# Kernel tuning notes

Hardware: AMD Instinct MI355X
Metric: run time of the kernel (lower is better)

The kernel has to match this reference:

```python
import jax, jax.numpy as jnp
import numpy as np

B, N, E, S, A, P, T = 512, 65536, 131072, 256, 512, 2, 64


def setup_inputs() -> dict:
    key = jax.random.key(0)
    ks = jax.random.split(key, 40)
    f32 = jnp.float32

    def g(i, shape, s=0.05):
        return jax.random.normal(ks[i], shape, f32) * s

    inp = {
        'nodes': jax.random.normal(ks[0], (N, S), f32),
        'edge_features': jax.random.normal(ks[1], (E, S), f32),
        'edge_source': jax.random.randint(ks[2], (E,), 0, N),
        'edge_dest': jax.random.randint(ks[3], (E,), 0, N),
        'node_owner': jax.random.randint(ks[4], (N,), 0, B),
        'running': jnp.ones((B,), bool),
        'ref_types': jax.random.randint(ks[5], (B,), 0, T),
        # decision aggregator (transform + sigmoid gate)
        'dec_t_W': g(6, (A, S)), 'dec_t_b': g(7, (A,)),
        'dec_g_W': g(8, (A, S)), 'dec_g_b': jnp.ones((A,), f32),
        # init aggregator
        'init_t_W': g(9, (A, S)), 'init_t_b': g(10, (A,)),
        'init_g_W': g(11, (A, S)), 'init_g_b': jnp.ones((A,), f32),
        # node type decision head + embedding
        'ntd_W': g(12, (T + 1, A)), 'ntd_b': g(13, (T + 1,)),
        'nte': g(14, (T, S), 1.0),
        # f_init
        'f1_W': g(15, (S, S)), 'f1_b': g(16, (S,)),
        'f2_W': g(17, (S, A)),
        # propagator params, stacked over P steps (message_size = 2S)
        'mn_W': g(18, (P, 2 * S, S)),
        'mf_W': g(19, (P, 2 * S, S)),
        'ml2_W': g(20, (P, 2 * S, 2 * S)), 'ml2_b': g(21, (P, 2 * S)),
        'gru_Wih': g(22, (P, 3 * S, 2 * S)), 'gru_Whh': g(23, (P, 3 * S, S)),
        'gru_bih': jnp.zeros((P, 3 * S), f32),
        'gru_bhh': jnp.concatenate(
            [jnp.ones((P, S), f32), jnp.zeros((P, 2 * S), f32)], axis=-1),
    }
    return inp


def _aggregate(nodes, fmask, tW, tb, gW, gb):
    # Aggregator.forward: sigmoid gate * linear transform, pooled per graph
    # via dense 0/1 owner-mask matmul (dropout=0 -> identity).
    gates = jax.nn.sigmoid(nodes @ gW.T + gb)
    data = nodes @ tW.T + tb
    return fmask @ (data * gates)  # [B, A]


def reference(nodes, edge_features, edge_source, edge_dest, node_owner,
              running, ref_types,
              dec_t_W, dec_t_b, dec_g_W, dec_g_b,
              init_t_W, init_t_b, init_g_W, init_g_b,
              ntd_W, ntd_b, nte, f1_W, f1_b, f2_W,
              mn_W, mf_W, ml2_W, ml2_b, gru_Wih, gru_Whh, gru_bih, gru_bhh):
    f32 = nodes.dtype
    fmask = (node_owner[None, :] == jnp.arange(B)[:, None]).astype(f32)  # [B,N]
    # Propagator._node_update_mask: owner_masks[running].sum(0) > 0
    upd = (fmask * running[:, None].astype(f32)).sum(0) > 0  # [N]

    for p in range(P):
        ef = edge_features @ mf_W[p].T                 # [E, 2S]
        nf = nodes @ mn_W[p].T                         # [N, 2S]
        msgs = nf[edge_source] + nf[edge_dest] + ef
        msgs = jnp.tanh(msgs) @ ml2_W[p].T + ml2_b[p]  # message_layer_2
        inputs = jnp.zeros((N, 2 * S), f32)
        inputs = inputs.at[edge_dest].add(msgs).at[edge_source].add(msgs)
        # torch GRUCell (gate order r, z, n)
        gi = inputs @ gru_Wih[p].T + gru_bih[p]
        gh = nodes @ gru_Whh[p].T + gru_bhh[p]
        ir, iz, inn = jnp.split(gi, 3, axis=-1)
        hr, hz, hn = jnp.split(gh, 3, axis=-1)
        r = jax.nn.sigmoid(ir + hr)
        z = jax.nn.sigmoid(iz + hz)
        n = jnp.tanh(inn + r * hn)
        new_nodes = (1.0 - z) * n + z * nodes
        nodes = jnp.where(upd[:, None], new_nodes, nodes)

    # node-type decision
    agg = _aggregate(nodes, fmask, dec_t_W, dec_t_b, dec_g_W, dec_g_b)
    logits = agg @ ntd_W.T + ntd_b                      # [B, T+1]

    # training path: remap_pad (no pad chars present) -> ref + 1
    sel = ref_types + 1                                  # in [1, T]
    logp = jax.nn.log_softmax(logits, axis=-1)
    per_ex = -logp[jnp.arange(B), sel]
    loss = jnp.where(running, per_ex, 0.0).mean()

    # new node features for running graphs
    emb = nte[sel - 1]                                   # [B, S]
    init_feats = _aggregate(nodes, fmask, init_t_W, init_t_b,
                            init_g_W, init_g_b)
    new_features = emb @ f1_W.T + f1_b + init_feats @ f2_W.T  # [B, S]
    return logits, new_features, loss
```

## Files before the change

### kernel.cpp

```cpp
#include <hip/hip_runtime.h>
#include <hip/hip_bf16.h>
#include <math.h>

#define BG 512
#define NN 65536
#define EE 131072
#define SD 256
#define AD 512
#define PP 2
#define TD 64

typedef __attribute__((ext_vector_type(8))) short sx8;
typedef __attribute__((ext_vector_type(4))) short sx4;
typedef __attribute__((ext_vector_type(4))) float fx4;

__device__ __forceinline__ float bs2f(short s) {
    union { unsigned u; float f; } x; x.u = ((unsigned)(unsigned short)s) << 16; return x.f;
}
__device__ __forceinline__ short f2bs(float f) {
    union { float f; unsigned u; } x; x.f = f;
    unsigned r = x.u + 0x7fffu + ((x.u >> 16) & 1u);
    return (short)(r >> 16);
}
__device__ __forceinline__ float fast_tanh(float x) {
    float xc = fminf(fmaxf(x, -15.f), 15.f);
    float e = __expf(2.f * xc);
    return __fdividef(e - 1.f, e + 1.f);
}
__device__ __forceinline__ float fast_sigm(float x) {
    float xc = fminf(fmaxf(x, -30.f), 30.f);
    float e = __expf(-xc);
    return __fdividef(1.f, 1.f + e);
}
__device__ __forceinline__ bool run_flag(const void* runv, int idx) {
    const unsigned char* r8 = (const unsigned char*)runv;
    const int* r32 = (const int*)runv;
    return (r8[idx] != 0) || (r32[idx] != 0);
}

__device__ __forceinline__ void gload16(const short* g, short* l) {
    __builtin_amdgcn_global_load_lds(
        (const __attribute__((address_space(1))) void*)g,
        (__attribute__((address_space(3))) void*)l, 16, 0, 0);
}

template<int EPI>
__launch_bounds__(256, 4)
__global__ void gemm_bt(const short* __restrict__ Abp, const short* __restrict__ Abp2,
                        const short* __restrict__ Wp,
                        const float* __restrict__ bias, const float* __restrict__ bias2,
                        short* __restrict__ Cout, short* __restrict__ Fout,
                        short* __restrict__ FoutB,
                        const float* __restrict__ biasB, const float* __restrict__ biasB2,
                        const int* __restrict__ degp,
                        int K, int Ksp, int NC, int NT, int nsplit)
{
    __shared__ __align__(16) short sA[2 * 4096];
    __shared__ __align__(16) short sB[2 * 4096];
    const int t = threadIdx.x;
    const int lane = t & 63;
    const int w = t >> 6;

    const int nwg = gridDim.x;
    const int q = nwg >> 3;
    const int wg = (blockIdx.x & 7) * q + (blockIdx.x >> 3);
    const int mt = wg / NT;
    const int nt = wg - mt * NT;
    const int m0 = mt * 128;
    const int n0 = nt * 128;

    const int wm = (w >> 1) * 64;
    const int wn = (w & 1) * 64;
    const int lr = lane & 15;
    const int lg = lane >> 4;

    fx4 acc[4][4];
#pragma unroll
    for (int i = 0; i < 4; i++)
#pragma unroll
        for (int j = 0; j < 4; j++) { fx4 z = {0.f, 0.f, 0.f, 0.f}; acc[i][j] = z; }

    const int r = t >> 2;
    const int cblk = (t & 3) ^ ((r >> 1) & 3);
    const short* gA  = Abp  + (size_t)(m0 + r) * Ksp + cblk * 8;
    const short* gA2 = Abp2 + (size_t)(m0 + r) * (K - Ksp) + cblk * 8;
    const short* gB  = Wp + (size_t)(n0 + r) * K + cblk * 8;
    const size_t rsA  = (size_t)64 * Ksp;
    const size_t rsA2 = (size_t)64 * (K - Ksp);
    const size_t rsB  = (size_t)64 * K;

    auto STAGE = [&](int b, int kk) {
        const short* a0 = (kk < Ksp) ? (gA + kk) : (gA2 + (kk - Ksp));
        const size_t rs = (kk < Ksp) ? rsA : rsA2;
        gload16(a0,            sA + b * 4096 + w * 512);
        gload16(a0 + rs,       sA + b * 4096 + 2048 + w * 512);
        gload16(gB + kk,       sB + b * 4096 + w * 512);
        gload16(gB + kk + rsB, sB + b * 4096 + 2048 + w * 512);
    };

    STAGE(0, 0);

    float dgv[4];
    if (EPI == 3) {
#pragma unroll
        for (int mi = 0; mi < 4; mi++)
            dgv[mi] = (float)degp[m0 + wm + mi * 16 + lr];
    }

    __syncthreads();
    int buf = 0;
    const int xa = (lr >> 1) & 3;
    for (int kk = 0; kk < K; kk += 32) {
        if (kk + 32 < K) STAGE(buf ^ 1, kk + 32);
        const short* cA = sA + buf * 4096;
        const short* cB = sB + buf * 4096;
        sx8 af[4], bfr[4];
#pragma unroll
        for (int mi = 0; mi < 4; mi++)
            af[mi] = *(const sx8*)(cA + (wm + mi * 16 + lr) * 32 + (lg ^ xa) * 8);
#pragma unroll
        for (int ni = 0; ni < 4; ni++)
            bfr[ni] = *(const sx8*)(cB + (wn + ni * 16 + lr) * 32 + (lg ^ xa) * 8);
#pragma unroll
        for (int mi = 0; mi < 4; mi++)
#pragma unroll
            for (int ni = 0; ni < 4; ni++) {
                if (EPI == 4)
                    acc[mi][ni] = __builtin_amdgcn_mfma_f32_16x16x32_bf16(
                        af[mi], bfr[ni], acc[mi][ni], 0, 0, 0);
                else
                    acc[mi][ni] = __builtin_amdgcn_mfma_f32_16x16x32_bf16(
                        bfr[ni], af[mi], acc[mi][ni], 0, 0, 0);
            }
        __syncthreads();
        buf ^= 1;
    }

    if (EPI == 4) {
        const bool useB = (n0 >= nsplit);
        short* fo = useB ? FoutB : Fout;
        const float* tb = useB ? biasB : bias;
        const float* gb = useB ? biasB2 : bias2;
        const int ln0 = useB ? (n0 - nsplit) : n0;
#pragma unroll
        for (int mi = 0; mi < 4; mi++) {
#pragma unroll
            for (int rg = 0; rg < 4; rg++) {
                const int m = m0 + wm + mi * 16 + lg * 4 + rg;
#pragma unroll
                for (int ni = 0; ni < 4; ni += 2) {
                    const int rc = (((ln0 + wn + ni * 16) >> 5) << 4) + lr;
                    float dv = acc[mi][ni][rg] + tb[rc];
                    float gv = fast_sigm(acc[mi][ni + 1][rg] + gb[rc]);
                    fo[(size_t)m * 512 + rc] = f2bs(dv * gv);
                }
            }
        }
    } else {
#pragma unroll
        for (int mi = 0; mi < 4; mi++) {
            const int m = m0 + wm + mi * 16 + lr;
            short* co = Cout + (size_t)m * NC + n0;
#pragma unroll
            for (int ni = 0; ni < 4; ni++) {
                const int nc = wn + ni * 16 + lg * 4;
                sx4 o;
                if (EPI == 1) {
#pragma unroll
                    for (int rg = 0; rg < 4; rg++)
                        o[rg] = f2bs(fast_tanh(acc[mi][ni][rg]));
                } else if (EPI == 3) {
                    fx4 bv = *(const fx4*)(bias + n0 + nc);
                    fx4 cv = *(const fx4*)(bias2 + n0 + nc);
#pragma unroll
                    for (int rg = 0; rg < 4; rg++)
                        o[rg] = f2bs(acc[mi][ni][rg] + dgv[mi] * cv[rg] + bv[rg]);
                } else {
                    fx4 vb = {0.f, 0.f, 0.f, 0.f};
                    if (bias) vb = *(const fx4*)(bias + n0 + nc);
#pragma unroll
                    for (int rg = 0; rg < 4; rg++)
                        o[rg] = f2bs(acc[mi][ni][rg] + vb[rg]);
                }
                *(sx4*)(co + nc) = o;
            }
        }
    }
}

__global__ void k_xadd(const short* __restrict__ nodes, const int* __restrict__ esrc,
                       const int* __restrict__ edst, short* __restrict__ X)
{
    size_t idx = ((size_t)blockIdx.x * 256 + threadIdx.x) * 8;
    const int e = (int)(idx >> 8);
    const int j = (int)(idx & 255);
    const int s = esrc[e], d = edst[e];
    sx8 a = *(const sx8*)(nodes + (size_t)s * 256 + j);
    sx8 b = *(const sx8*)(nodes + (size_t)d * 256 + j);
    sx8 o;
#pragma unroll
    for (int u = 0; u < 8; u++) o[u] = f2bs(bs2f(a[u]) + bs2f(b[u]));
    *(sx8*)(X + idx) = o;
}

__global__ void k_castw(const float* __restrict__ in, short* __restrict__ out)
{
    size_t i = ((size_t)blockIdx.x * 256 + threadIdx.x) * 4;
    fx4 v = *(const fx4*)(in + i);
    sx4 o;
#pragma unroll
    for (int u = 0; u < 4; u++) o[u] = f2bs(v[u]);
    *(sx4*)(out + i) = o;
}

__global__ void k_cast_T(const float* __restrict__ in, short* __restrict__ out)
{
    size_t i = ((size_t)blockIdx.x * 256 + threadIdx.x) * 4;
    const int k = (int)(i >> 9);
    const int k2 = (int)(i & 511);
    sx4 o;
#pragma unroll
    for (int u = 0; u < 4; u++) o[u] = f2bs(in[(size_t)(k2 + u) * 512 + k]);
    *(sx4*)(out + i) = o;
}

__global__ void k_vecfuse(const float* __restrict__ Wih, const float* __restrict__ ml2b,
                          float* __restrict__ c1)
{
    const int i = blockIdx.x * 256 + threadIdx.x;
    if (i >= 768) return;
    const float* wr = Wih + (size_t)i * 512;
    float acc = 0.f;
    for (int k = 0; k < 512; k++) acc += wr[k] * ml2b[k];
    c1[i] = acc;
}

__global__ void k_fill_gru(const short* __restrict__ Whh, short* __restrict__ out)
{
    size_t idx = ((size_t)blockIdx.x * 256 + threadIdx.x) * 4;
    const int o = (int)(idx / 768);
    const int k = (int)(idx % 768);
    if (o < 768 && k < 512) return;
    sx4 v = {0, 0, 0, 0};
    if (k >= 512) {
        if (o < 512)       v = *(const sx4*)(Whh + (size_t)o * 256 + (k - 512));
        else if (o >= 768) v = *(const sx4*)(Whh + (size_t)(o - 256) * 256 + (k - 512));
    }
    *(sx4*)(out + idx) = v;
}

__global__ void k_grubias(const float* __restrict__ bih, const float* __restrict__ bhh,
                          const float* __restrict__ c1,
                          float* __restrict__ bg, float* __restrict__ cg)
{
    const int o = blockIdx.x * 256 + threadIdx.x;
    if (o >= 1024) return;
    float b, c;
    if (o < 512)      { b = bih[o] + bhh[o]; c = c1[o]; }
    else if (o < 768) { b = bih[o];          c = c1[o]; }
    else              { b = bhh[o - 256];    c = 0.f;   }
    bg[o] = b; cg[o] = c;
}

__global__ void k_cast_comb(const float* __restrict__ mn, const float* __restrict__ mf,
                            short* __restrict__ out)
{
    size_t i = ((size_t)blockIdx.x * 256 + threadIdx.x) * 4;
    const int n = (int)(i >> 9);
    const int k = (int)(i & 511);
    const float* W = (k < 256) ? (mn + (size_t)n * 256 + k)
                               : (mf + (size_t)n * 256 + (k - 256));
    fx4 v = *(const fx4*)W;
    sx4 o;
#pragma unroll
    for (int u = 0; u < 4; u++) o[u] = f2bs(v[u]);
    *(sx4*)(out + i) = o;
}

__global__ void k_cast_pair(const float* __restrict__ tW, const float* __restrict__ gW,
                            short* __restrict__ out)
{
    size_t i = ((size_t)blockIdx.x * 256 + threadIdx.x) * 4;
    const int r2 = (int)(i >> 8);
    const int c = (int)(i & 255);
    const int src = ((r2 >> 5) << 4) | (r2 & 15);
    const float* W = ((r2 >> 4) & 1) ? gW : tW;
    fx4 v = *(const fx4*)(W + (size_t)src * 256 + c);
    sx4 o;
#pragma unroll
    for (int u = 0; u < 4; u++) o[u] = f2bs(v[u]);
    *(sx4*)(out + i) = o;
}

__global__ void k_count2(const int* __restrict__ a, const int* __restrict__ b,
                         int* __restrict__ deg, int n)
{
    int i = blockIdx.x * 256 + threadIdx.x;
    if (i < n) { atomicAdd(&deg[a[i]], 1); atomicAdd(&deg[b[i]], 1); }
}
__global__ void k_count1(const int* __restrict__ a, int* __restrict__ deg, int n)
{
    int i = blockIdx.x * 256 + threadIdx.x;
    if (i < n) atomicAdd(&deg[a[i]], 1);
}
__global__ void k_scan(const int* __restrict__ deg, int* __restrict__ offs, int n)
{
    __shared__ int part[256];
    const int t = threadIdx.x;
    const int chunk = n >> 8;
    const int base = t * chunk;
    int s = 0;
    for (int i = 0; i < chunk; i++) s += deg[base + i];
    part[t] = s;
    __syncthreads();
    for (int off = 1; off < 256; off <<= 1) {
        int v = (t >= off) ? part[t - off] : 0;
        __syncthreads();
        part[t] += v;
        __syncthreads();
    }
    int run = (t > 0) ? part[t - 1] : 0;
    for (int i = 0; i < chunk; i++) {
        offs[base + i] = run;
        run += deg[base + i];
    }
    if (t == 255) offs[n] = part[255];
}
__global__ void k_fill2(const int* __restrict__ a, const int* __restrict__ b,
                        const int* __restrict__ offs, int* __restrict__ cur,
                        int* __restrict__ elist, int n)
{
    int i = blockIdx.x * 256 + threadIdx.x;
    if (i < n) {
        int p = atomicAdd(&cur[a[i]], 1); elist[offs[a[i]] + p] = i;
        int q = atomicAdd(&cur[b[i]], 1); elist[offs[b[i]] + q] = i;
    }
}
__global__ void k_fill1(const int* __restrict__ own, const int* __restrict__ offs,
                        int* __restrict__ cur, int* __restrict__ nlist, int n)
{
    int i = blockIdx.x * 256 + threadIdx.x;
    if (i < n) {
        int p = atomicAdd(&cur[own[i]], 1); nlist[offs[own[i]] + p] = i;
    }
}

__global__ void k_edge_gather(const short* __restrict__ msgs, const int* __restrict__ offs,
                              const int* __restrict__ elist, short* __restrict__ inp)
{
    const int node = blockIdx.x * 4 + (threadIdx.x >> 6);
    const int c = (threadIdx.x & 63) * 8;
    const int s0 = offs[node], s1 = offs[node + 1];
    float acc[8] = {0.f, 0.f, 0.f, 0.f, 0.f, 0.f, 0.f, 0.f};
    for (int s = s0; s < s1; s++) {
        const int e = elist[s];
        sx8 v = *(const sx8*)(msgs + (size_t)e * 512 + c);
#pragma unroll
        for (int u = 0; u < 8; u++) acc[u] += bs2f(v[u]);
    }
    sx8 o;
#pragma unroll
    for (int u = 0; u < 8; u++) o[u] = f2bs(acc[u]);
    *(sx8*)(inp + (size_t)node * 512 + c) = o;
}

__global__ void k_owner_reduce(const short* __restrict__ gp, const int* __restrict__ offsB,
                               const int* __restrict__ nlist, float* __restrict__ agg)
{
    const int b = blockIdx.x, t = threadIdx.x;
    const int s0 = offsB[b], s1 = offsB[b + 1];
    float a0 = 0.f, a1 = 0.f;
    for (int s = s0; s < s1; s++) {
        const int n = nlist[s];
        const short* pp = gp + (size_t)n * 512 + t * 2;
        a0 += bs2f(pp[0]); a1 += bs2f(pp[1]);
    }
    agg[(size_t)b * 512 + t * 2] = a0;
    agg[(size_t)b * 512 + t * 2 + 1] = a1;
}

__global__ void k_gru(const short* __restrict__ G, short* __restrict__ nodes,
                      const int* __restrict__ owner, const void* __restrict__ runv)
{
    const int n = blockIdx.x * 4 + (threadIdx.x >> 6);
    const int t = threadIdx.x & 63;
    const bool run = run_flag(runv, owner[n]);
    const size_t gb = (size_t)n * 1024 + t * 4;
    sx4 grr = *(const sx4*)(G + gb);
    sx4 grz = *(const sx4*)(G + gb + 256);
    sx4 gin = *(const sx4*)(G + gb + 512);
    sx4 ghn = *(const sx4*)(G + gb + 768);
    const size_t nbase = (size_t)n * 256 + t * 4;
    sx4 old4 = *(const sx4*)(nodes + nbase);
    sx4 outb;
#pragma unroll
    for (int u = 0; u < 4; u++) {
        float old = bs2f(old4[u]);
        float rr = fast_sigm(bs2f(grr[u]));
        float zz = fast_sigm(bs2f(grz[u]));
        float nn = fast_tanh(bs2f(gin[u]) + rr * bs2f(ghn[u]));
        float nv = (1.f - zz) * nn + zz * old;
        outb[u] = run ? f2bs(nv) : old4[u];
    }
    *(sx4*)(nodes + nbase) = outb;
}

__global__ void k_logits(const float* __restrict__ agg, const float* __restrict__ Wt,
                         const float* __restrict__ bt, float* __restrict__ logitsF,
                         float* __restrict__ outL)
{
    __shared__ float row[512];
    const int b = blockIdx.x, t = threadIdx.x;
    for (int k = t; k < 512; k += 128) row[k] = agg[(size_t)b * 512 + k];
    __syncthreads();
    if (t < TD + 1) {
        float acc = bt[t];
        const float* wr = Wt + (size_t)t * 512;
        for (int k = 0; k < 512; k++) acc += row[k] * wr[k];
        logitsF[b * (TD + 1) + t] = acc;
        outL[b * (TD + 1) + t] = acc;
    }
}

__global__ void k_loss(const float* __restrict__ logitsF, const int* __restrict__ reft,
                       const void* __restrict__ runv, float* __restrict__ outLoss)
{
    __shared__ float red[512];
    const int b = threadIdx.x;
    const float* lr = logitsF + b * (TD + 1);
    float mx = lr[0];
    for (int k = 1; k < TD + 1; k++) mx = fmaxf(mx, lr[k]);
    float se = 0.f;
    for (int k = 0; k < TD + 1; k++) se += expf(lr[k] - mx);
    const int sel = reft[b] + 1;
    float pe = logf(se) + mx - lr[sel];
    red[b] = run_flag(runv, b) ? pe : 0.f;
    __syncthreads();
    for (int s = 256; s > 0; s >>= 1) {
        if (b < s) red[b] += red[b + s];
        __syncthreads();
    }
    if (b == 0) outLoss[0] = red[0] / (float)BG;
}

__global__ void k_newfeat(const float* __restrict__ aggi, const float* __restrict__ nte,
                          const int* __restrict__ reft, const float* __restrict__ f1W,
                          const float* __restrict__ f1b, const float* __restrict__ f2W,
                          float* __restrict__ outNF)
{
    __shared__ float emb[256];
    __shared__ float ag[512];
    const int b = blockIdx.x, t = threadIdx.x;
    const int rt = reft[b];
    emb[t] = nte[(size_t)rt * 256 + t];
    ag[t] = aggi[(size_t)b * 512 + t];
    ag[t + 256] = aggi[(size_t)b * 512 + 256 + t];
    __syncthreads();
    float acc = f1b[t];
    const float* w1 = f1W + (size_t)t * 256;
    for (int k = 0; k < 256; k++) acc += emb[k] * w1[k];
    const float* w2 = f2W + (size_t)t * 512;
    for (int a = 0; a < 512; a++) acc += ag[a] * w2[a];
    outNF[(size_t)b * 256 + t] = acc;
}

extern "C" void kernel_launch(void* const* d_in, const int* in_sizes, int n_in,
                              void* d_out, int out_size, void* d_ws, size_t ws_size,
                              hipStream_t stream)
{
    (void)in_sizes; (void)n_in; (void)out_size;
    const float* in_nodes = (const float*)d_in[0];
    const float* in_ef    = (const float*)d_in[1];
    const int*   e_src    = (const int*)d_in[2];
    const int*   e_dst    = (const int*)d_in[3];
    const int*   owner    = (const int*)d_in[4];
    const void*  running  = d_in[5];
    const int*   reft     = (const int*)d_in[6];
    const float* dec_tW = (const float*)d_in[7];
    const float* dec_tb = (const float*)d_in[8];
    const float* dec_gW = (const float*)d_in[9];
    const float* dec_gb = (const float*)d_in[10];
    const float* init_tW = (const float*)d_in[11];
    const float* init_tb = (const float*)d_in[12];
    const float* init_gW = (const float*)d_in[13];
    const float* init_gb = (const float*)d_in[14];
    const float* ntdW = (const float*)d_in[15];
    const float* ntdb = (const float*)d_in[16];
    const float* nte  = (const float*)d_in[17];
    const float* f1W  = (const float*)d_in[18];
    const float* f1b  = (const float*)d_in[19];
    const float* f2W  = (const float*)d_in[20];
    const float* mnW  = (const float*)d_in[21];
    const float* mfW  = (const float*)d_in[22];
    const float* ml2W = (const float*)d_in[23];
    const float* ml2b = (const float*)d_in[24];
    const float* Wih  = (const float*)d_in[25];
    const float* Whh  = (const float*)d_in[26];
    const float* bih  = (const float*)d_in[27];
    const float* bhh  = (const float*)d_in[28];

    float* outL    = (float*)d_out;
    float* outNF   = outL + BG * (TD + 1);
    float* outLoss = outNF + BG * SD;

    size_t off = 0;
    auto take = [&](size_t bytes) -> void* {
        void* p = (char*)d_ws + off;
        off += (bytes + 255) & ~(size_t)255;
        return p;
    };
    short* nodes_bf  = (short*)take((size_t)NN * SD * 2);
    short* ef_bf     = (short*)take((size_t)EE * SD * 2);
    short* bufC      = (short*)take((size_t)EE * SD * 2);
    short* bufD      = (short*)take((size_t)EE * 512 * 2);
    short* bufM      = (short*)take((size_t)EE * 512 * 2);
    short* bufI      = (short*)take((size_t)NN * 512 * 2);
    float* aggD      = (float*)take((size_t)BG * AD * 4);
    float* aggI      = (float*)take((size_t)BG * AD * 4);
    float* logitsF   = (float*)take((size_t)BG * (TD + 1) * 4);
    short* WcombB = (short*)take((size_t)PP * 512 * 512 * 2);
    short* ml2Tb  = (short*)take((size_t)512 * 512 * 2);
    short* WgruB  = (short*)take((size_t)PP * 1024 * 768 * 2);
    float* c1f    = (float*)take((size_t)PP * 768 * 4);
    float* bgru   = (float*)take((size_t)PP * 1024 * 4);
    float* cgru   = (float*)take((size_t)PP * 1024 * 4);
    short* WihB  = (short*)take((size_t)PP * 768 * 512 * 2);
    short* WhhB  = (short*)take((size_t)PP * 768 * 256 * 2);
    short* W4agg = (short*)take((size_t)2048 * 256 * 2);
    int* deg_e = (int*)take((size_t)NN * 4);
    int* offs_e = (int*)take((size_t)(NN + 1) * 4);
    int* cur_e = (int*)take((size_t)NN * 4);
    int* elist = (int*)take((size_t)2 * EE * 4);
    int* degB = (int*)take((size_t)BG * 4);
    int* offsB = (int*)take((size_t)(BG + 1) * 4);
    int* curB = (int*)take((size_t)BG * 4);
    int* nlist = (int*)take((size_t)NN * 4);
    if (off > ws_size) return;

    short* G   = bufD;
    short* gpD = bufM;
    short* gpI = bufD;

    k_castw<<<NN * SD / 1024, 256, 0, stream>>>(in_nodes, nodes_bf);
    k_castw<<<EE * SD / 1024, 256, 0, stream>>>(in_ef, ef_bf);
    for (int p = 0; p < PP; p++)
        k_cast_comb<<<512 * 512 / 1024, 256, 0, stream>>>(
            mnW + (size_t)p * 512 * 256, mfW + (size_t)p * 512 * 256,
            WcombB + (size_t)p * 512 * 512);
    k_castw<<<PP * 768 * 512 / 1024, 256, 0, stream>>>(Wih, WihB);
    k_castw<<<PP * 768 * 256 / 1024, 256, 0, stream>>>(Whh, WhhB);
    k_cast_pair<<<1024 * 256 / 1024, 256, 0, stream>>>(dec_tW, dec_gW, W4agg);
    k_cast_pair<<<1024 * 256 / 1024, 256, 0, stream>>>(init_tW, init_gW,
                                                       W4agg + 1024 * 256);
    for (int p = 0; p < PP; p++) {
        k_cast_T<<<512 * 512 / 1024, 256, 0, stream>>>(
            ml2W + (size_t)p * 512 * 512, ml2Tb);
        gemm_bt<0><<<768 / 128 * 4, 256, 0, stream>>>(
            WihB + (size_t)p * 768 * 512, WihB + (size_t)p * 768 * 512, ml2Tb,
            nullptr, nullptr, WgruB + (size_t)p * 1024 * 768,
            nullptr, nullptr, nullptr, nullptr, nullptr,
            512, 512, 768, 4, 0);
        k_vecfuse<<<3, 256, 0, stream>>>(Wih + (size_t)p * 768 * 512,
                                         ml2b + (size_t)p * 512, c1f + p * 768);
        k_fill_gru<<<1024 * 768 / 4 / 256, 256, 0, stream>>>(
            WhhB + (size_t)p * 768 * 256, WgruB + (size_t)p * 1024 * 768);
        k_grubias<<<4, 256, 0, stream>>>(bih + (size_t)p * 768, bhh + (size_t)p * 768,
                                         c1f + p * 768, bgru + p * 1024, cgru + p * 1024);
    }

    hipMemsetAsync(deg_e, 0, (size_t)NN * 4, stream);
    hipMemsetAsync(cur_e, 0, (size_t)NN * 4, stream);
    hipMemsetAsync(degB, 0, (size_t)BG * 4, stream);
    hipMemsetAsync(curB, 0, (size_t)BG * 4, stream);
    k_count2<<<(EE + 255) / 256, 256, 0, stream>>>(e_src, e_dst, deg_e, EE);
    k_scan<<<1, 256, 0, stream>>>(deg_e, offs_e, NN);
    k_fill2<<<(EE + 255) / 256, 256, 0, stream>>>(e_src, e_dst, offs_e, cur_e, elist, EE);
    k_count1<<<(NN + 255) / 256, 256, 0, stream>>>(owner, degB, NN);
    k_scan<<<1, 256, 0, stream>>>(degB, offsB, BG);
    k_fill1<<<(NN + 255) / 256, 256, 0, stream>>>(owner, offsB, curB, nlist, NN);

    for (int p = 0; p < PP; p++) {
        k_xadd<<<EE / 8, 256, 0, stream>>>(nodes_bf, e_src, e_dst, bufC);
        gemm_bt<1><<<EE / 128 * 4, 256, 0, stream>>>(
            bufC, ef_bf, WcombB + (size_t)p * 512 * 512, nullptr, nullptr,
            bufD, nullptr, nullptr, nullptr, nullptr, nullptr,
            512, 256, 512, 4, 0);
        k_edge_gather<<<NN / 4, 256, 0, stream>>>(bufD, offs_e, elist, bufI);
        gemm_bt<3><<<NN / 128 * 8, 256, 0, stream>>>(
            bufI, nodes_bf, WgruB + (size_t)p * 1024 * 768,
            bgru + p * 1024, cgru + p * 1024,
            G, nullptr, nullptr, nullptr, nullptr, deg_e,
            768, 512, 1024, 8, 0);
        k_gru<<<NN / 4, 256, 0, stream>>>(G, nodes_bf, owner, running);
    }

    gemm_bt<4><<<NN / 128 * 16, 256, 0, stream>>>(
        nodes_bf, nodes_bf, W4agg, dec_tb, dec_gb,
        nullptr, gpD, gpI, init_tb, init_gb, nullptr,
        256, 256, 2048, 16, 1024);
    k_owner_reduce<<<BG, 256, 0, stream>>>(gpD, offsB, nlist, aggD);
    k_owner_reduce<<<BG, 256, 0, stream>>>(gpI, offsB, nlist, aggI);

    k_logits<<<BG, 128, 0, stream>>>(aggD, ntdW, ntdb, logitsF, outL);
    k_loss<<<1, 512, 0, stream>>>(logitsF, reft, running, outLoss);
    k_newfeat<<<BG, 256, 0, stream>>>(aggI, nte, reft, f1W, f1b, f2W, outNF);
}
```

Baseline: 1.626 ms.

## Fuse GRU cell into gate GEMM epilogue with interleaved weight rows

Reorders the fused GRU weight and bias rows so the r, z, n-input and n-hidden columns for each feature sit next to each other within a thread's accumulator quad. The GEMM epilogue can then apply the GRU nonlinearity and the running mask directly, writing the new bf16 node state. This drops the separate k_gru kernel and the round trip of the 1024-wide gate tensor G. Node state is ping-ponged between two buffers because the epilogue reads the old state while writing the new one; the epilogue now does narrower scalar stores.

```diff
diff --git a/kernel.cpp b/kernel.cpp
--- a/kernel.cpp
+++ b/kernel.cpp
@@ -53,6 +53,8 @@
                         short* __restrict__ FoutB,
                         const float* __restrict__ biasB, const float* __restrict__ biasB2,
                         const int* __restrict__ degp,
+                        const short* __restrict__ oldp, const int* __restrict__ ownp,
+                        const void* __restrict__ runv,
                         int K, int Ksp, int NC, int NT, int nsplit)
 {
     __shared__ __align__(16) short sA[2 * 4096];
@@ -101,10 +103,14 @@
     STAGE(0, 0);
 
     float dgv[4];
-    if (EPI == 3) {
-#pragma unroll
-        for (int mi = 0; mi < 4; mi++)
-            dgv[mi] = (float)degp[m0 + wm + mi * 16 + lr];
+    bool rn[4];
+    if (EPI == 5) {
+#pragma unroll
+        for (int mi = 0; mi < 4; mi++) {
+            const int m = m0 + wm + mi * 16 + lr;
+            dgv[mi] = (float)degp[m];
+            rn[mi] = run_flag(runv, ownp[m]);
+        }
     }
 
     __syncthreads();
@@ -156,6 +162,29 @@
                 }
             }
         }
+    } else if (EPI == 5) {
+#pragma unroll
+        for (int mi = 0; mi < 4; mi++) {
+            const int m = m0 + wm + mi * 16 + lr;
+#pragma unroll
+            for (int ni = 0; ni < 4; ni++) {
+                const int cbase = n0 + wn + ni * 16 + lg * 4;
+                const int s = cbase >> 2;
+                fx4 bv = *(const fx4*)(bias + cbase);
+                fx4 cv = *(const fx4*)(bias2 + cbase);
+                float v0 = acc[mi][ni][0] + dgv[mi] * cv[0] + bv[0];
+                float v1 = acc[mi][ni][1] + dgv[mi] * cv[1] + bv[1];
+                float v2 = acc[mi][ni][2] + dgv[mi] * cv[2] + bv[2];
+                float v3 = acc[mi][ni][3] + dgv[mi] * cv[3] + bv[3];
+                float rr = fast_sigm(v0);
+                float zz = fast_sigm(v1);
+                float nn = fast_tanh(v2 + rr * v3);
+                const size_t oidx = (size_t)m * 256 + s;
+                short oldb = oldp[oidx];
+                float nv = (1.f - zz) * nn + zz * bs2f(oldb);
+                Cout[oidx] = rn[mi] ? f2bs(nv) : oldb;
+            }
+        }
     } else {
 #pragma unroll
         for (int mi = 0; mi < 4; mi++) {
@@ -169,12 +198,6 @@
 #pragma unroll
                     for (int rg = 0; rg < 4; rg++)
                         o[rg] = f2bs(fast_tanh(acc[mi][ni][rg]));
-                } else if (EPI == 3) {
-                    fx4 bv = *(const fx4*)(bias + n0 + nc);
-                    fx4 cv = *(const fx4*)(bias2 + n0 + nc);
-#pragma unroll
-                    for (int rg = 0; rg < 4; rg++)
-                        o[rg] = f2bs(acc[mi][ni][rg] + dgv[mi] * cv[rg] + bv[rg]);
                 } else {
                     fx4 vb = {0.f, 0.f, 0.f, 0.f};
                     if (bias) vb = *(const fx4*)(bias + n0 + nc);
@@ -235,31 +258,38 @@
     c1[i] = acc;
 }
 
-__global__ void k_fill_gru(const short* __restrict__ Whh, short* __restrict__ out)
+__global__ void k_fill_gru4(const short* __restrict__ WfB, const short* __restrict__ Whh,
+                            short* __restrict__ out)
 {
     size_t idx = ((size_t)blockIdx.x * 256 + threadIdx.x) * 4;
-    const int o = (int)(idx / 768);
+    const int rp = (int)(idx / 768);
     const int k = (int)(idx % 768);
-    if (o < 768 && k < 512) return;
+    const int s = rp >> 2, c = rp & 3;
     sx4 v = {0, 0, 0, 0};
-    if (k >= 512) {
-        if (o < 512)       v = *(const sx4*)(Whh + (size_t)o * 256 + (k - 512));
-        else if (o >= 768) v = *(const sx4*)(Whh + (size_t)(o - 256) * 256 + (k - 512));
+    if (k < 512) {
+        if (c < 3) v = *(const sx4*)(WfB + (size_t)(c * 256 + s) * 512 + k);
+    } else {
+        if (c != 2) {
+            const int o = (c == 3 ? 512 : c * 256) + s;
+            v = *(const sx4*)(Whh + (size_t)o * 256 + (k - 512));
+        }
     }
     *(sx4*)(out + idx) = v;
 }
 
-__global__ void k_grubias(const float* __restrict__ bih, const float* __restrict__ bhh,
-                          const float* __restrict__ c1,
-                          float* __restrict__ bg, float* __restrict__ cg)
-{
-    const int o = blockIdx.x * 256 + threadIdx.x;
-    if (o >= 1024) return;
-    float b, c;
-    if (o < 512)      { b = bih[o] + bhh[o]; c = c1[o]; }
-    else if (o < 768) { b = bih[o];          c = c1[o]; }
-    else              { b = bhh[o - 256];    c = 0.f;   }
-    bg[o] = b; cg[o] = c;
+__global__ void k_grubias4(const float* __restrict__ bih, const float* __restrict__ bhh,
+                           const float* __restrict__ c1,
+                           float* __restrict__ bg, float* __restrict__ cg)
+{
+    const int rp = blockIdx.x * 256 + threadIdx.x;
+    if (rp >= 1024) return;
+    const int s = rp >> 2, c = rp & 3;
+    float b, cc;
+    if (c == 0)      { b = bih[s] + bhh[s];             cc = c1[s]; }
+    else if (c == 1) { b = bih[256 + s] + bhh[256 + s]; cc = c1[256 + s]; }
+    else if (c == 2) { b = bih[512 + s];                cc = c1[512 + s]; }
+    else             { b = bhh[512 + s];                cc = 0.f; }
+    bg[rp] = b; cg[rp] = cc;
 }
 
 __global__ void k_cast_comb(const float* __restrict__ mn, const float* __restrict__ mf,
@@ -377,32 +407,6 @@
     }
     agg[(size_t)b * 512 + t * 2] = a0;
     agg[(size_t)b * 512 + t * 2 + 1] = a1;
-}
-
-__global__ void k_gru(const short* __restrict__ G, short* __restrict__ nodes,
-                      const int* __restrict__ owner, const void* __restrict__ runv)
-{
-    const int n = blockIdx.x * 4 + (threadIdx.x >> 6);
-    const int t = threadIdx.x & 63;
-    const bool run = run_flag(runv, owner[n]);
-    const size_t gb = (size_t)n * 1024 + t * 4;
-    sx4 grr = *(const sx4*)(G + gb);
-    sx4 grz = *(const sx4*)(G + gb + 256);
-    sx4 gin = *(const sx4*)(G + gb + 512);
-    sx4 ghn = *(const sx4*)(G + gb + 768);
-    const size_t nbase = (size_t)n * 256 + t * 4;
-    sx4 old4 = *(const sx4*)(nodes + nbase);
-    sx4 outb;
-#pragma unroll
-    for (int u = 0; u < 4; u++) {
-        float old = bs2f(old4[u]);
-        float rr = fast_sigm(bs2f(grr[u]));
-        float zz = fast_sigm(bs2f(grz[u]));
-        float nn = fast_tanh(bs2f(gin[u]) + rr * bs2f(ghn[u]));
-        float nv = (1.f - zz) * nn + zz * old;
-        outb[u] = run ? f2bs(nv) : old4[u];
-    }
-    *(sx4*)(nodes + nbase) = outb;
 }
 
 __global__ void k_logits(const float* __restrict__ agg, const float* __restrict__ Wt,
@@ -509,18 +513,19 @@
         off += (bytes + 255) & ~(size_t)255;
         return p;
     };
-    short* nodes_bf  = (short*)take((size_t)NN * SD * 2);
+    short* nodesA    = (short*)take((size_t)NN * SD * 2);
+    short* nodesB    = (short*)take((size_t)NN * SD * 2);
     short* ef_bf     = (short*)take((size_t)EE * SD * 2);
     short* bufC      = (short*)take((size_t)EE * SD * 2);
     short* bufD      = (short*)take((size_t)EE * 512 * 2);
-    short* bufM      = (short*)take((size_t)EE * 512 * 2);
     short* bufI      = (short*)take((size_t)NN * 512 * 2);
     float* aggD      = (float*)take((size_t)BG * AD * 4);
     float* aggI      = (float*)take((size_t)BG * AD * 4);
     float* logitsF   = (float*)take((size_t)BG * (TD + 1) * 4);
     short* WcombB = (short*)take((size_t)PP * 512 * 512 * 2);
     short* ml2Tb  = (short*)take((size_t)512 * 512 * 2);
-    short* WgruB  = (short*)take((size_t)PP * 1024 * 768 * 2);
+    short* WfB    = (short*)take((size_t)768 * 512 * 2);
+    short* Wgru4  = (short*)take((size_t)PP * 1024 * 768 * 2);
     float* c1f    = (float*)take((size_t)PP * 768 * 4);
     float* bgru   = (float*)take((size_t)PP * 1024 * 4);
     float* cgru   = (float*)take((size_t)PP * 1024 * 4);
@@ -537,11 +542,10 @@
     int* nlist = (int*)take((size_t)NN * 4);
     if (off > ws_size) return;
 
-    short* G   = bufD;
-    short* gpD = bufM;
+    short* gpD = bufI;
     short* gpI = bufD;
 
-    k_castw<<<NN * SD / 1024, 256, 0, stream>>>(in_nodes, nodes_bf);
+    k_castw<<<NN * SD / 1024, 256, 0, stream>>>(in_nodes, nodesA);
     k_castw<<<EE * SD / 1024, 256, 0, stream>>>(in_ef, ef_bf);
     for (int p = 0; p < PP; p++)
         k_cast_comb<<<512 * 512 / 1024, 256, 0, stream>>>(
@@ -557,15 +561,15 @@
             ml2W + (size_t)p * 512 * 512, ml2Tb);
         gemm_bt<0><<<768 / 128 * 4, 256, 0, stream>>>(
             WihB + (size_t)p * 768 * 512, WihB + (size_t)p * 768 * 512, ml2Tb,
-            nullptr, nullptr, WgruB + (size_t)p * 1024 * 768,
-            nullptr, nullptr, nullptr, nullptr, nullptr,
-            512, 512, 768, 4, 0);
+            nullptr, nullptr, WfB, nullptr, nullptr, nullptr, nullptr,
+            nullptr, nullptr, nullptr, nullptr,
+            512, 512, 512, 4, 0);
         k_vecfuse<<<3, 256, 0, stream>>>(Wih + (size_t)p * 768 * 512,
                                          ml2b + (size_t)p * 512, c1f + p * 768);
-        k_fill_gru<<<1024 * 768 / 4 / 256, 256, 0, stream>>>(
-            WhhB + (size_t)p * 768 * 256, WgruB + (size_t)p * 1024 * 768);
-        k_grubias<<<4, 256, 0, stream>>>(bih + (size_t)p * 768, bhh + (size_t)p * 768,
-                                         c1f + p * 768, bgru + p * 1024, cgru + p * 1024);
+        k_fill_gru4<<<1024 * 768 / 4 / 256, 256, 0, stream>>>(
+            WfB, WhhB + (size_t)p * 768 * 256, Wgru4 + (size_t)p * 1024 * 768);
+        k_grubias4<<<4, 256, 0, stream>>>(bih + (size_t)p * 768, bhh + (size_t)p * 768,
+                                          c1f + p * 768, bgru + p * 1024, cgru + p * 1024);
     }
 
     hipMemsetAsync(deg_e, 0, (size_t)NN * 4, stream);
@@ -580,23 +584,27 @@
     k_fill1<<<(NN + 255) / 256, 256, 0, stream>>>(owner, offsB, curB, nlist, NN);
 
     for (int p = 0; p < PP; p++) {
-        k_xadd<<<EE / 8, 256, 0, stream>>>(nodes_bf, e_src, e_dst, bufC);
+        short* cur = (p & 1) ? nodesB : nodesA;
+        short* nxt = (p & 1) ? nodesA : nodesB;
+        k_xadd<<<EE / 8, 256, 0, stream>>>(cur, e_src, e_dst, bufC);
         gemm_bt<1><<<EE / 128 * 4, 256, 0, stream>>>(
             bufC, ef_bf, WcombB + (size_t)p * 512 * 512, nullptr, nullptr,
-            bufD, nullptr, nullptr, nullptr, nullptr, nullptr,
+            bufD, nullptr, nullptr, nullptr, nullptr,
+            nullptr, nullptr, nullptr, nullptr,
             512, 256, 512, 4, 0);
         k_edge_gather<<<NN / 4, 256, 0, stream>>>(bufD, offs_e, elist, bufI);
-        gemm_bt<3><<<NN / 128 * 8, 256, 0, stream>>>(
-            bufI, nodes_bf, WgruB + (size_t)p * 1024 * 768,
+        gemm_bt<5><<<NN / 128 * 8, 256, 0, stream>>>(
+            bufI, cur, Wgru4 + (size_t)p * 1024 * 768,
             bgru + p * 1024, cgru + p * 1024,
-            G, nullptr, nullptr, nullptr, nullptr, deg_e,
+            nxt, nullptr, nullptr, nullptr, nullptr,
+            deg_e, cur, owner, running,
             768, 512, 1024, 8, 0);
-        k_gru<<<NN / 4, 256, 0, stream>>>(G, nodes_bf, owner, running);
     }
 
     gemm_bt<4><<<NN / 128 * 16, 256, 0, stream>>>(
-        nodes_bf, nodes_bf, W4agg, dec_tb, dec_gb,
-        nullptr, gpD, gpI, init_tb, init_gb, nullptr,
+        nodesA, nodesA, W4agg, dec_tb, dec_gb,
+        nullptr, gpD, gpI, init_tb, init_gb,
+        nullptr, nullptr, nullptr, nullptr,
         256, 256, 2048, 16, 1024);
     k_owner_reduce<<<BG, 256, 0, stream>>>(gpD, offsB, nlist, aggD);
     k_owner_reduce<<<BG, 256, 0, stream>>>(gpI, offsB, nlist, aggI);
```

Result: no change. 1.607 ms (-1.2%).
